# Kernel optimization log

Measured on AMD Instinct MI355X. Metric: run time of the kernel, lower is better.

## Reference

```python
import jax, jax.numpy as jnp
import numpy as np

N_HEAD, D_MODEL, D_K, D_V = 16, 1024, 64, 64
B, S = 4, 2048
LN_EPS = 1e-5

def setup_inputs() -> dict:
    key = jax.random.key(0)
    ks = jax.random.split(key, 12)
    s = 1.0 / np.sqrt(D_MODEL)
    x = jax.random.normal(ks[0], (B, S, D_MODEL), dtype=jnp.float32)
    Wq = jax.random.normal(ks[1], (N_HEAD, D_MODEL, D_K), dtype=jnp.float32) * s
    bq = jax.random.normal(ks[2], (N_HEAD, D_K), dtype=jnp.float32) * 0.01
    Wk = jax.random.normal(ks[3], (N_HEAD, D_MODEL, D_K), dtype=jnp.float32) * s
    bk = jax.random.normal(ks[4], (N_HEAD, D_K), dtype=jnp.float32) * 0.01
    Wv = jax.random.normal(ks[5], (N_HEAD, D_MODEL, D_V), dtype=jnp.float32) * s
    bv = jax.random.normal(ks[6], (N_HEAD, D_V), dtype=jnp.float32) * 0.01
    Wfc = jax.random.normal(ks[7], (N_HEAD * D_V, D_MODEL), dtype=jnp.float32) * (1.0 / np.sqrt(N_HEAD * D_V))
    bfc = jax.random.normal(ks[8], (D_MODEL,), dtype=jnp.float32) * 0.01
    gamma = jnp.ones((D_MODEL,), dtype=jnp.float32)
    beta = jnp.zeros((D_MODEL,), dtype=jnp.float32)
    return {"x": x, "Wq": Wq, "bq": bq, "Wk": Wk, "bk": bk, "Wv": Wv, "bv": bv,
            "Wfc": Wfc, "bfc": bfc, "gamma": gamma, "beta": beta}

def reference(x, Wq, bq, Wk, bk, Wv, bv, Wfc, bfc, gamma, beta):
    # Per-head projections batched over heads: [B,H,S,d]
    q = jnp.einsum('bsd,hdk->bhsk', x, Wq) + bq[None, :, None, :]
    k = jnp.einsum('bsd,hdk->bhsk', x, Wk) + bk[None, :, None, :]
    v = jnp.einsum('bsd,hdv->bhsv', x, Wv) + bv[None, :, None, :]
    scores = jnp.einsum('bhqk,bhsk->bhqs', q, k) / jnp.sqrt(jnp.float32(D_K))
    probs = jax.nn.softmax(scores, axis=-1)
    attn = jnp.einsum('bhqs,bhsv->bhqv', probs, v)  # [B,H,S,Dv]
    # concat heads (cat along last dim == transpose heads to feature axis)
    cat = attn.transpose(0, 2, 1, 3).reshape(B, S, N_HEAD * D_V)
    y = cat @ Wfc + bfc
    mu = jnp.mean(y, axis=-1, keepdims=True)
    var = jnp.mean(jnp.square(y - mu), axis=-1, keepdims=True)
    return (y - mu) * jax.lax.rsqrt(var + LN_EPS) * gamma + beta
```

## Files before the change

kernel.cpp:

```cpp
#include <hip/hip_runtime.h>

#define NH 16
#define DMODEL 1024
#define DK 64
#define DV 64
#define BB 4
#define SS 2048
#define NTOK (BB*SS)
#define LN_EPS 1e-5f
#define SM_SHIFT 13.0f

typedef __attribute__((ext_vector_type(4))) float f32x4;
typedef __attribute__((ext_vector_type(8))) short s16x8;
typedef __attribute__((ext_vector_type(4))) short s16x4;

__device__ __forceinline__ short f2bf(float f) {
    union { float f; unsigned u; } a; a.f = f;
    unsigned r = a.u + 0x7FFFu + ((a.u >> 16) & 1u);
    return (short)(r >> 16);
}
__device__ __forceinline__ unsigned pk2(float a, float b) {
    union { float f; unsigned u; } x, y; x.f = a; y.f = b;
    return __builtin_amdgcn_perm(x.u + 0x8000u, y.u + 0x8000u, 0x07060302u);
}
__device__ __forceinline__ float fexp2(float x) { return __builtin_amdgcn_exp2f(x); }
__device__ __forceinline__ void gll16(const void* g, void* l) {
    __builtin_amdgcn_global_load_lds(
        (const __attribute__((address_space(1))) unsigned int*)g,
        (__attribute__((address_space(3))) unsigned int*)l, 16, 0, 0);
}

__global__ void k_cast_x(const float* __restrict__ x, short* __restrict__ xb) {
    int i = blockIdx.x * blockDim.x + threadIdx.x;
    f32x4 v = reinterpret_cast<const f32x4*>(x)[i];
    s16x4 o;
    o[0] = f2bf(v[0]); o[1] = f2bf(v[1]); o[2] = f2bf(v[2]); o[3] = f2bf(v[3]);
    reinterpret_cast<s16x4*>(xb)[i] = o;
}

__global__ __launch_bounds__(256) void k_conv_wqkv_t(const float* __restrict__ Wq,
                                                     const float* __restrict__ Wk,
                                                     const float* __restrict__ Wv,
                                                     short* __restrict__ WT) {
    __shared__ float tile[64][17];
    const int mh = blockIdx.y;
    const int mat = mh >> 4, h = mh & 15;
    const int dt = blockIdx.x >> 2, kt = blockIdx.x & 3;
    const float* src = (mat == 0 ? Wq : (mat == 1 ? Wk : Wv));
    const int t = threadIdx.x;
    #pragma unroll
    for (int p = 0; p < 4; p++) {
        int d = p * 16 + (t >> 4), kk = t & 15;
        tile[d][kk] = src[((size_t)h * 1024 + dt * 64 + d) * 64 + kt * 16 + kk];
    }
    __syncthreads();
    #pragma unroll
    for (int p = 0; p < 4; p++) {
        int kk = p * 4 + (t >> 6), d = t & 63;
        WT[((size_t)mat * 1024 + h * 64 + kt * 16 + kk) * 1024 + dt * 64 + d] = f2bf(tile[d][kk]);
    }
}

__global__ __launch_bounds__(256) void k_conv_wfc_t(const float* __restrict__ Wfc,
                                                    short* __restrict__ WfcT) {
    __shared__ float tile[64][17];
    const int ct = blockIdx.x >> 6, nt = blockIdx.x & 63;
    const int t = threadIdx.x;
    #pragma unroll
    for (int p = 0; p < 4; p++) {
        int c = p * 16 + (t >> 4), n = t & 15;
        tile[c][n] = Wfc[((size_t)ct * 64 + c) * 1024 + nt * 16 + n];
    }
    __syncthreads();
    #pragma unroll
    for (int p = 0; p < 4; p++) {
        int n = p * 4 + (t >> 6), c = t & 63;
        WfcT[((size_t)nt * 16 + n) * 1024 + ct * 64 + c] = f2bf(tile[c][n]);
    }
}

template<int MODE, int NBX, int NWG>
__global__ __launch_bounds__(256) void k_gemm2(const short* __restrict__ A,
                                               const short* __restrict__ BT,
                                               const float* __restrict__ bq,
                                               const float* __restrict__ bk,
                                               const float* __restrict__ bv,
                                               const float* __restrict__ bfc,
                                               short* __restrict__ Qb,
                                               short* __restrict__ Kb,
                                               short* __restrict__ Vt,
                                               short* __restrict__ Yb) {
    __shared__ short smem[2][128][64];
    const int fid = blockIdx.x + blockIdx.y * NBX;
    const int swzid = (fid & 7) * (NWG / 8) + (fid >> 3);
    const int gm0 = (swzid / NBX) * 128, gn0 = (swzid % NBX) * 128;
    const int t = threadIdx.x, lane = t & 63, w = t >> 6;
    const int wm = w >> 1, wn = w & 1;
    const int lr = lane & 15, lg = lane >> 4;

    f32x4 acc[4][4] = {};

    const int lrow = t >> 3, gl = t & 7;
    const int sgx = (gl ^ (lrow & 7)) << 3;
    const short* pa = A  + (size_t)(gm0 + lrow) * 1024 + sgx;
    const short* pb = BT + (size_t)(gn0 + lrow) * 1024 + sgx;
    char* dA = (char*)smem[0] + w * 1024;
    char* dB = (char*)smem[1] + w * 1024;

    const int x7 = lr & 7;
    const int gx0 = (lg ^ x7) << 4;
    const int gx1 = ((4 + lg) ^ x7) << 4;

    for (int k0 = 0; k0 < 1024; k0 += 64) {
        #pragma unroll
        for (int c = 0; c < 4; c++) {
            gll16(pa + (size_t)c * 32768 + k0, dA + c * 4096);
            gll16(pb + (size_t)c * 32768 + k0, dB + c * 4096);
        }
        __syncthreads();
        s16x8 aF[2][4], bF[2][4];
        #pragma unroll
        for (int i = 0; i < 4; i++) {
            const char* rpa = (char*)smem[0] + (wm * 64 + i * 16 + lr) * 128;
            const char* rpb = (char*)smem[1] + (wn * 64 + i * 16 + lr) * 128;
            aF[0][i] = *(const s16x8*)(rpa + gx0);
            aF[1][i] = *(const s16x8*)(rpa + gx1);
            bF[0][i] = *(const s16x8*)(rpb + gx0);
            bF[1][i] = *(const s16x8*)(rpb + gx1);
        }
        __builtin_amdgcn_s_setprio(1);
        #pragma unroll
        for (int kk = 0; kk < 2; kk++)
            #pragma unroll
            for (int i = 0; i < 4; i++)
                #pragma unroll
                for (int j = 0; j < 4; j++)
                    acc[i][j] = __builtin_amdgcn_mfma_f32_16x16x32_bf16(aF[kk][i], bF[kk][j], acc[i][j], 0, 0, 0);
        __builtin_amdgcn_s_setprio(0);
        __syncthreads();
    }

    short (*ct)[128] = (short(*)[128])smem;
    const float* bias; int nloc0; float scale = 1.0f;
    if (MODE == 0) {
        if (gn0 < 1024)      { bias = bq; nloc0 = gn0;        scale = 0.18033688011112042f; }
        else if (gn0 < 2048) { bias = bk; nloc0 = gn0 - 1024; }
        else                 { bias = bv; nloc0 = gn0 - 2048; }
    } else { bias = bfc; nloc0 = gn0; }
    float bval[4];
    #pragma unroll
    for (int j = 0; j < 4; j++) bval[j] = bias[nloc0 + wn * 64 + j * 16 + lr];

    #pragma unroll
    for (int i = 0; i < 4; i++)
        #pragma unroll
        for (int j = 0; j < 4; j++) {
            const int colg = wn * 4 + j;
            #pragma unroll
            for (int rg = 0; rg < 4; rg++) {
                int row = wm * 64 + i * 16 + lg * 4 + rg;
                int cg = colg ^ ((row >> 1) & 7);
                ct[row][(cg << 4) + lr] = f2bf((acc[i][j][rg] + bval[j]) * scale);
            }
        }
    __syncthreads();

    if (MODE == 0 && gn0 >= 2048) {
        const int s0 = gm0 & 2047;
        const int b2v = gm0 >> 11;
        const int cg16 = lane >> 4;
        const int l16 = lane & 15;
        #pragma unroll
        for (int step = 0; step < 8; step++) {
            int c = w * 32 + step * 4 + cg16;
            int nl = (gn0 - 2048) + c;
            int h2 = nl >> 6, v = nl & 63;
            s16x8 o;
            #pragma unroll
            for (int j = 0; j < 8; j++) {
                int p = l16 * 8 + j;
                int blk = p >> 5, g = (p >> 3) & 3, h16 = (p >> 2) & 1, i2 = p & 3;
                int row = blk * 32 + h16 * 16 + g * 4 + i2;
                int cg2 = (c >> 4) ^ ((row >> 1) & 7);
                o[j] = ct[row][(cg2 << 4) + (c & 15)];
            }
            *(s16x8*)(Vt + ((size_t)(b2v * NH + h2) * 64 + v) * SS + s0 + l16 * 8) = o;
        }
    } else {
        short* dstM = (MODE == 0) ? (gn0 < 1024 ? Qb : Kb) : Yb;
        #pragma unroll
        for (int rr = 0; rr < 2; rr++) {
            const int row = w * 16 + (lane >> 2) + rr * 64;
            const int m = gm0 + row;
            const int swz = (row >> 1) & 7;
            #pragma unroll
            for (int j = 0; j < 4; j++) {
                const int c = (lane & 3) + j * 4;
                const int cg = (c >> 1) ^ swz;
                s16x8 v = *(const s16x8*)((char*)ct + row * 256 + (cg << 5) + (c & 1) * 16);
                if (MODE == 0) {
                    int b2 = m >> 11, s2 = m & 2047;
                    int n0 = (gn0 & 1023) + c * 8;
                    int h2 = n0 >> 6, kk = n0 & 63;
                    *(s16x8*)(dstM + ((size_t)(b2 * NH + h2) * SS + s2) * DK + kk) = v;
                } else {
                    *(s16x8*)(dstM + (size_t)m * 1024 + gn0 + c * 8) = v;
                }
            }
        }
    }
}

__global__ __launch_bounds__(512) void k_attn2(const short* __restrict__ Qb,
                                               const short* __restrict__ Kb,
                                               const short* __restrict__ VT2,
                                               short* __restrict__ cat) {
    __shared__ char smem[2][16384];
    const int fid = blockIdx.x + blockIdx.y * gridDim.x;
    const int swz = ((fid & 7) << 6) | (fid >> 3);
    const int qt = swz & 7, bh = swz >> 3;
    const int b = bh >> 4, h = bh & 15;
    const int t = threadIdx.x, lane = t & 63, w = t >> 6;
    const int lr = lane & 15, lg = lane >> 4;

    const short* Qbase = Qb + ((size_t)bh * SS + qt * 256 + w * 32) * DK;
    s16x8 qF[2][2];
    #pragma unroll
    for (int f = 0; f < 2; f++) {
        qF[f][0] = *(const s16x8*)(Qbase + (f * 16 + lr) * DK + lg * 8);
        qF[f][1] = *(const s16x8*)(Qbase + (f * 16 + lr) * DK + 32 + lg * 8);
    }
    s16x8 onesF;
    #pragma unroll
    for (int i = 0; i < 8; i++) onesF[i] = (short)0x3F80;

    const char* Kbase = (const char*)(Kb + (size_t)bh * SS * DK);
    const char* Vbase = (const char*)(VT2 + (size_t)bh * DK * SS);
    const int rk = w * 8 + (lane >> 3);
    const int gl = lane & 7;
    const char* pK = Kbase + rk * 128 + ((gl ^ (rk & 7)) << 4);
    const char* pV = Vbase + rk * (SS * 2) + ((gl ^ (rk & 7)) << 4);

    const int x7 = lr & 7;
    const int gx0 = (lg ^ x7) << 4;
    const int gx1 = ((4 + lg) ^ x7) << 4;

    f32x4 acc[2][4] = {};
    f32x4 accs[2] = {};
    const f32x4 zinit = {-SM_SHIFT, -SM_SHIFT, -SM_SHIFT, -SM_SHIFT};

    {
        char* d = smem[0];
        gll16(pK, d + w * 1024);
        gll16(pV, d + 8192 + w * 1024);
    }
    __syncthreads();

    int cur = 0;
    for (int kt = 0; kt < SS; kt += 64) {
        if (kt + 64 < SS) {
            char* d = smem[cur ^ 1];
            gll16(pK + (kt + 64) * 128, d + w * 1024);
            gll16(pV + (kt + 64) * 2,   d + 8192 + w * 1024);
        }
        const char* bs = smem[cur];

        s16x8 kA[4][2];
        #pragma unroll
        for (int kg = 0; kg < 4; kg++) {
            const char* rp = bs + (kg * 16 + lr) * 128;
            kA[kg][0] = *(const s16x8*)(rp + gx0);
            kA[kg][1] = *(const s16x8*)(rp + gx1);
        }
        f32x4 st[2][4];
        __builtin_amdgcn_s_setprio(1);
        #pragma unroll
        for (int f = 0; f < 2; f++)
            #pragma unroll
            for (int kg = 0; kg < 4; kg++) {
                f32x4 z = __builtin_amdgcn_mfma_f32_16x16x32_bf16(kA[kg][0], qF[f][0], zinit, 0, 0, 0);
                st[f][kg] = __builtin_amdgcn_mfma_f32_16x16x32_bf16(kA[kg][1], qF[f][1], z, 0, 0, 0);
            }
        __builtin_amdgcn_s_setprio(0);

        s16x8 pb[2][2];
        #pragma unroll
        for (int f = 0; f < 2; f++) {
            float p[4][4];
            #pragma unroll
            for (int kg = 0; kg < 4; kg++)
                #pragma unroll
                for (int rg = 0; rg < 4; rg++)
                    p[kg][rg] = fexp2(st[f][kg][rg]);
            #pragma unroll
            for (int ks = 0; ks < 2; ks++) {
                union { s16x8 v; unsigned u[4]; } U;
                U.u[0] = pk2(p[2 * ks][1],     p[2 * ks][0]);
                U.u[1] = pk2(p[2 * ks][3],     p[2 * ks][2]);
                U.u[2] = pk2(p[2 * ks + 1][1], p[2 * ks + 1][0]);
                U.u[3] = pk2(p[2 * ks + 1][3], p[2 * ks + 1][2]);
                pb[f][ks] = U.v;
            }
        }

        __builtin_amdgcn_s_setprio(1);
        #pragma unroll
        for (int f = 0; f < 2; f++) {
            accs[f] = __builtin_amdgcn_mfma_f32_16x16x32_bf16(onesF, pb[f][0], accs[f], 0, 0, 0);
            accs[f] = __builtin_amdgcn_mfma_f32_16x16x32_bf16(onesF, pb[f][1], accs[f], 0, 0, 0);
        }
        #pragma unroll
        for (int vt = 0; vt < 4; vt++) {
            const char* rp = bs + 8192 + (vt * 16 + lr) * 128;
            s16x8 vA0 = *(const s16x8*)(rp + gx0);
            s16x8 vA1 = *(const s16x8*)(rp + gx1);
            #pragma unroll
            for (int f = 0; f < 2; f++) {
                acc[f][vt] = __builtin_amdgcn_mfma_f32_16x16x32_bf16(vA0, pb[f][0], acc[f][vt], 0, 0, 0);
                acc[f][vt] = __builtin_amdgcn_mfma_f32_16x16x32_bf16(vA1, pb[f][1], acc[f][vt], 0, 0, 0);
            }
        }
        __builtin_amdgcn_s_setprio(0);
        __syncthreads();
        cur ^= 1;
    }

    char* ods = (char*)smem + w * 4096;
    float inv[2] = {1.0f / accs[0][0], 1.0f / accs[1][0]};
    #pragma unroll
    for (int f = 0; f < 2; f++)
        #pragma unroll
        for (int vt = 0; vt < 4; vt++)
            #pragma unroll
            for (int rg = 0; rg < 4; rg++)
                *(short*)(ods + (f * 16 + lr) * 128 + (vt * 16 + lg * 4 + rg) * 2) =
                    f2bf(acc[f][vt][rg] * inv[f]);
    __syncthreads();
    {
        int r = lane >> 1, hb = lane & 1;
        const char* srow = (char*)smem + w * 4096 + r * 128 + hb * 64;
        int token = b * SS + qt * 256 + w * 32 + r;
        char* dst = (char*)(cat + (size_t)token * 1024 + h * 64 + hb * 32);
        #pragma unroll
        for (int i = 0; i < 4; i++)
            *(s16x8*)(dst + i * 16) = *(const s16x8*)(srow + i * 16);
    }
}

__global__ __launch_bounds__(256) void k_ln(const short* __restrict__ Yb,
                                            const float* __restrict__ gamma,
                                            const float* __restrict__ beta,
                                            float* __restrict__ out) {
    const int row = blockIdx.x;
    const int t = threadIdx.x;
    s16x4 raw = reinterpret_cast<const s16x4*>(Yb + (size_t)row * 1024)[t];
    float v[4];
    #pragma unroll
    for (int i = 0; i < 4; i++) {
        union { unsigned u; float f; } cvt;
        cvt.u = ((unsigned)(unsigned short)raw[i]) << 16;
        v[i] = cvt.f;
    }
    float s = v[0] + v[1] + v[2] + v[3];
    float s2 = v[0] * v[0] + v[1] * v[1] + v[2] * v[2] + v[3] * v[3];
    #pragma unroll
    for (int off = 32; off; off >>= 1) {
        s += __shfl_xor(s, off);
        s2 += __shfl_xor(s2, off);
    }
    __shared__ float red[8];
    int w = t >> 6, lane = t & 63;
    if (lane == 0) { red[w] = s; red[4 + w] = s2; }
    __syncthreads();
    float S = red[0] + red[1] + red[2] + red[3];
    float S2 = red[4] + red[5] + red[6] + red[7];
    float mu = S * (1.f / 1024.f);
    float var = S2 * (1.f / 1024.f) - mu * mu;
    float rs = rsqrtf(var + LN_EPS);
    f32x4 g = reinterpret_cast<const f32x4*>(gamma)[t];
    f32x4 be = reinterpret_cast<const f32x4*>(beta)[t];
    f32x4 o;
    #pragma unroll
    for (int i = 0; i < 4; i++) o[i] = (v[i] - mu) * rs * g[i] + be[i];
    reinterpret_cast<f32x4*>(out + (size_t)row * 1024)[t] = o;
}

extern "C" void kernel_launch(void* const* d_in, const int* in_sizes, int n_in,
                              void* d_out, int out_size, void* d_ws, size_t ws_size,
                              hipStream_t stream) {
    const float* x    = (const float*)d_in[0];
    const float* Wq   = (const float*)d_in[1];
    const float* bq   = (const float*)d_in[2];
    const float* Wk   = (const float*)d_in[3];
    const float* bk   = (const float*)d_in[4];
    const float* Wv   = (const float*)d_in[5];
    const float* bv   = (const float*)d_in[6];
    const float* Wfc  = (const float*)d_in[7];
    const float* bfc  = (const float*)d_in[8];
    const float* gamma= (const float*)d_in[9];
    const float* beta = (const float*)d_in[10];
    float* out = (float*)d_out;

    char* p = (char*)d_ws;
    short* xb   = (short*)p; p += (size_t)NTOK * 1024 * 2;
    short* WT   = (short*)p; p += (size_t)3072 * 1024 * 2;
    short* WfcT = (short*)p; p += (size_t)1024 * 1024 * 2;
    short* Qb   = (short*)p; p += (size_t)64 * SS * 64 * 2;
    short* Kb   = (short*)p; p += (size_t)64 * SS * 64 * 2;
    short* Vb   = (short*)p; p += (size_t)64 * SS * 64 * 2;
    short* VTb  = (short*)p; p += (size_t)64 * 64 * SS * 2;
    short* cat  = (short*)p; p += (size_t)NTOK * 1024 * 2;
    short* Yb   = Qb;
    (void)Vb;

    k_cast_x     <<<NTOK * 1024 / 4 / 256, 256, 0, stream>>>(x, xb);
    k_conv_wqkv_t<<<dim3(64, 48), 256, 0, stream>>>(Wq, Wk, Wv, WT);
    k_conv_wfc_t <<<1024, 256, 0, stream>>>(Wfc, WfcT);
    k_gemm2<0, 24, 1536><<<dim3(24, 64), 256, 0, stream>>>(xb, WT, bq, bk, bv, nullptr, Qb, Kb, VTb, nullptr);
    k_attn2      <<<dim3(8, 64), 512, 0, stream>>>(Qb, Kb, VTb, cat);
    k_gemm2<1, 8, 512><<<dim3(8, 64), 256, 0, stream>>>(cat, WfcT, nullptr, nullptr, nullptr, bfc, nullptr, nullptr, nullptr, Yb);
    k_ln         <<<NTOK, 256, 0, stream>>>(Yb, gamma, beta, out);
}
```

Before: 183.9 us.

## Halve per-wave query rows in attention kernel and double the grid

Each wave in the attention kernel now processes 16 query rows instead of 32, so a block covers 128 queries and the grid doubles to 1024 blocks. This cuts accumulator and score registers per wave and gives more blocks to spread across the CUs, aiming for better occupancy and load balance. In exchange, K/V tiles are loaded from global/LDS twice as often per query, which lowers data reuse.

New measurement: 192.1 us. 4.5% more time.

```diff
diff --git a/kernel.cpp b/kernel.cpp
--- a/kernel.cpp
+++ b/kernel.cpp
@@ -217,19 +217,15 @@
                                                short* __restrict__ cat) {
     __shared__ char smem[2][16384];
     const int fid = blockIdx.x + blockIdx.y * gridDim.x;
-    const int swz = ((fid & 7) << 6) | (fid >> 3);
-    const int qt = swz & 7, bh = swz >> 3;
+    const int swz = ((fid & 7) << 7) | (fid >> 3);
+    const int qt = swz & 15, bh = swz >> 4;
     const int b = bh >> 4, h = bh & 15;
     const int t = threadIdx.x, lane = t & 63, w = t >> 6;
     const int lr = lane & 15, lg = lane >> 4;
 
-    const short* Qbase = Qb + ((size_t)bh * SS + qt * 256 + w * 32) * DK;
-    s16x8 qF[2][2];
-    #pragma unroll
-    for (int f = 0; f < 2; f++) {
-        qF[f][0] = *(const s16x8*)(Qbase + (f * 16 + lr) * DK + lg * 8);
-        qF[f][1] = *(const s16x8*)(Qbase + (f * 16 + lr) * DK + 32 + lg * 8);
-    }
+    const short* Qbase = Qb + ((size_t)bh * SS + qt * 128 + w * 16) * DK;
+    s16x8 qF0 = *(const s16x8*)(Qbase + lr * DK + lg * 8);
+    s16x8 qF1 = *(const s16x8*)(Qbase + lr * DK + 32 + lg * 8);
     s16x8 onesF;
     #pragma unroll
     for (int i = 0; i < 8; i++) onesF[i] = (short)0x3F80;
@@ -245,8 +241,8 @@
     const int gx0 = (lg ^ x7) << 4;
     const int gx1 = ((4 + lg) ^ x7) << 4;
 
-    f32x4 acc[2][4] = {};
-    f32x4 accs[2] = {};
+    f32x4 acc[4] = {};
+    f32x4 accs = {};
     const f32x4 zinit = {-SM_SHIFT, -SM_SHIFT, -SM_SHIFT, -SM_SHIFT};
 
     {
@@ -272,78 +268,63 @@
             kA[kg][0] = *(const s16x8*)(rp + gx0);
             kA[kg][1] = *(const s16x8*)(rp + gx1);
         }
-        f32x4 st[2][4];
+        f32x4 st[4];
         __builtin_amdgcn_s_setprio(1);
         #pragma unroll
-        for (int f = 0; f < 2; f++)
+        for (int kg = 0; kg < 4; kg++) {
+            f32x4 z = __builtin_amdgcn_mfma_f32_16x16x32_bf16(kA[kg][0], qF0, zinit, 0, 0, 0);
+            st[kg] = __builtin_amdgcn_mfma_f32_16x16x32_bf16(kA[kg][1], qF1, z, 0, 0, 0);
+        }
+        __builtin_amdgcn_s_setprio(0);
+
+        float p[4][4];
+        #pragma unroll
+        for (int kg = 0; kg < 4; kg++)
             #pragma unroll
-            for (int kg = 0; kg < 4; kg++) {
-                f32x4 z = __builtin_amdgcn_mfma_f32_16x16x32_bf16(kA[kg][0], qF[f][0], zinit, 0, 0, 0);
-                st[f][kg] = __builtin_amdgcn_mfma_f32_16x16x32_bf16(kA[kg][1], qF[f][1], z, 0, 0, 0);
-            }
-        __builtin_amdgcn_s_setprio(0);
-
-        s16x8 pb[2][2];
-        #pragma unroll
-        for (int f = 0; f < 2; f++) {
-            float p[4][4];
-            #pragma unroll
-            for (int kg = 0; kg < 4; kg++)
-                #pragma unroll
-                for (int rg = 0; rg < 4; rg++)
-                    p[kg][rg] = fexp2(st[f][kg][rg]);
-            #pragma unroll
-            for (int ks = 0; ks < 2; ks++) {
-                union { s16x8 v; unsigned u[4]; } U;
-                U.u[0] = pk2(p[2 * ks][1],     p[2 * ks][0]);
-                U.u[1] = pk2(p[2 * ks][3],     p[2 * ks][2]);
-                U.u[2] = pk2(p[2 * ks + 1][1], p[2 * ks + 1][0]);
-                U.u[3] = pk2(p[2 * ks + 1][3], p[2 * ks + 1][2]);
-                pb[f][ks] = U.v;
-            }
+            for (int rg = 0; rg < 4; rg++)
+                p[kg][rg] = fexp2(st[kg][rg]);
+        s16x8 pb[2];
+        #pragma unroll
+        for (int ks = 0; ks < 2; ks++) {
+            union { s16x8 v; unsigned u[4]; } U;
+            U.u[0] = pk2(p[2 * ks][1],     p[2 * ks][0]);
+            U.u[1] = pk2(p[2 * ks][3],     p[2 * ks][2]);
+            U.u[2] = pk2(p[2 * ks + 1][1], p[2 * ks + 1][0]);
+            U.u[3] = pk2(p[2 * ks + 1][3], p[2 * ks + 1][2]);
+            pb[ks] = U.v;
         }
 
         __builtin_amdgcn_s_setprio(1);
-        #pragma unroll
-        for (int f = 0; f < 2; f++) {
-            accs[f] = __builtin_amdgcn_mfma_f32_16x16x32_bf16(onesF, pb[f][0], accs[f], 0, 0, 0);
-            accs[f] = __builtin_amdgcn_mfma_f32_16x16x32_bf16(onesF, pb[f][1], accs[f], 0, 0, 0);
-        }
+        accs = __builtin_amdgcn_mfma_f32_16x16x32_bf16(onesF, pb[0], accs, 0, 0, 0);
+        accs = __builtin_amdgcn_mfma_f32_16x16x32_bf16(onesF, pb[1], accs, 0, 0, 0);
         #pragma unroll
         for (int vt = 0; vt < 4; vt++) {
             const char* rp = bs + 8192 + (vt * 16 + lr) * 128;
             s16x8 vA0 = *(const s16x8*)(rp + gx0);
             s16x8 vA1 = *(const s16x8*)(rp + gx1);
-            #pragma unroll
-            for (int f = 0; f < 2; f++) {
-                acc[f][vt] = __builtin_amdgcn_mfma_f32_16x16x32_bf16(vA0, pb[f][0], acc[f][vt], 0, 0, 0);
-                acc[f][vt] = __builtin_amdgcn_mfma_f32_16x16x32_bf16(vA1, pb[f][1], acc[f][vt], 0, 0, 0);
-            }
+            acc[vt] = __builtin_amdgcn_mfma_f32_16x16x32_bf16(vA0, pb[0], acc[vt], 0, 0, 0);
+            acc[vt] = __builtin_amdgcn_mfma_f32_16x16x32_bf16(vA1, pb[1], acc[vt], 0, 0, 0);
         }
         __builtin_amdgcn_s_setprio(0);
         __syncthreads();
         cur ^= 1;
     }
 
-    char* ods = (char*)smem + w * 4096;
-    float inv[2] = {1.0f / accs[0][0], 1.0f / accs[1][0]};
-    #pragma unroll
-    for (int f = 0; f < 2; f++)
-        #pragma unroll
-        for (int vt = 0; vt < 4; vt++)
-            #pragma unroll
-            for (int rg = 0; rg < 4; rg++)
-                *(short*)(ods + (f * 16 + lr) * 128 + (vt * 16 + lg * 4 + rg) * 2) =
-                    f2bf(acc[f][vt][rg] * inv[f]);
+    char* ods = (char*)smem + w * 2048;
+    float inv = 1.0f / accs[0];
+    #pragma unroll
+    for (int vt = 0; vt < 4; vt++)
+        #pragma unroll
+        for (int rg = 0; rg < 4; rg++)
+            *(short*)(ods + lr * 128 + (vt * 16 + lg * 4 + rg) * 2) = f2bf(acc[vt][rg] * inv);
     __syncthreads();
     {
-        int r = lane >> 1, hb = lane & 1;
-        const char* srow = (char*)smem + w * 4096 + r * 128 + hb * 64;
-        int token = b * SS + qt * 256 + w * 32 + r;
-        char* dst = (char*)(cat + (size_t)token * 1024 + h * 64 + hb * 32);
-        #pragma unroll
-        for (int i = 0; i < 4; i++)
-            *(s16x8*)(dst + i * 16) = *(const s16x8*)(srow + i * 16);
+        int r = lane >> 2, hb = lane & 3;
+        const char* srow = (char*)smem + w * 2048 + r * 128 + hb * 32;
+        int token = b * SS + qt * 128 + w * 16 + r;
+        char* dst = (char*)(cat + (size_t)token * 1024 + h * 64 + hb * 16);
+        *(s16x8*)(dst)      = *(const s16x8*)(srow);
+        *(s16x8*)(dst + 16) = *(const s16x8*)(srow + 16);
     }
 }
 
@@ -417,7 +398,7 @@
     k_conv_wqkv_t<<<dim3(64, 48), 256, 0, stream>>>(Wq, Wk, Wv, WT);
     k_conv_wfc_t <<<1024, 256, 0, stream>>>(Wfc, WfcT);
     k_gemm2<0, 24, 1536><<<dim3(24, 64), 256, 0, stream>>>(xb, WT, bq, bk, bv, nullptr, Qb, Kb, VTb, nullptr);
-    k_attn2      <<<dim3(8, 64), 512, 0, stream>>>(Qb, Kb, VTb, cat);
+    k_attn2      <<<dim3(16, 64), 512, 0, stream>>>(Qb, Kb, VTb, cat);
     k_gemm2<1, 8, 512><<<dim3(8, 64), 256, 0, stream>>>(cat, WfcT, nullptr, nullptr, nullptr, bfc, nullptr, nullptr, nullptr, Yb);
     k_ln         <<<NTOK, 256, 0, stream>>>(Yb, gamma, beta, out);
 }
```

## Split QKV projection into 256x256-tile GEMM for Q/K and existing kernel for V

Applied to the files above, without the earlier changes.

The Q and K columns of the fused QKV projection move to a new 512-thread GEMM that uses 256x256 output tiles, explicit double-buffered LDS staging with direct global-to-LDS loads, and MFMA priority hints. The V part stays on the old 128x128 kernel, now launched with a column offset so it writes the transposed V layout. Larger tiles are meant to raise arithmetic intensity and cut global traffic for the Q/K projection. The cost is an extra kernel launch, higher LDS and register pressure, and fewer workgroups for the Q/K part (256 blocks).

After: 179.4 us. -2.4%, faster.

```diff
diff --git a/kernel.cpp b/kernel.cpp
--- a/kernel.cpp
+++ b/kernel.cpp
@@ -79,7 +79,139 @@
     }
 }
 
-template<int MODE, int NBX, int NWG>
+__global__ __launch_bounds__(512, 2) void k_gemm3(const short* __restrict__ A,
+                                                  const short* __restrict__ BT,
+                                                  const float* __restrict__ bq,
+                                                  const float* __restrict__ bk,
+                                                  short* __restrict__ Qb,
+                                                  short* __restrict__ Kb) {
+    __shared__ short lds[2][2][256][64];
+    const int fid = blockIdx.x + blockIdx.y * 8;
+    const int swz = (fid & 7) * 32 + (fid >> 3);
+    const int gm0 = (swz >> 3) * 256, gn0 = (swz & 7) * 256;
+    const int t = threadIdx.x, lane = t & 63, w = t >> 6;
+    const int wm = w >> 2, wn = w & 3;
+    const int lr = lane & 15, lg = lane >> 4;
+
+    f32x4 acc[8][4] = {};
+
+    const int lrow = t >> 3, gl = t & 7;
+    const int sgx = (gl ^ (lrow & 7)) << 3;
+    const short* pa = A  + (size_t)(gm0 + lrow) * 1024 + sgx;
+    const short* pb = BT + (size_t)(gn0 + lrow) * 1024 + sgx;
+
+    const int x7 = lr & 7;
+    const int gx0 = (lg ^ x7) << 4;
+    const int gx1 = ((4 + lg) ^ x7) << 4;
+
+    char* a0 = (char*)lds[0][0]; char* b0 = (char*)lds[0][1];
+    char* a1 = (char*)lds[1][0]; char* b1 = (char*)lds[1][1];
+
+    auto STAGE = [&](int k0, char* dA, char* dB) {
+        #pragma unroll
+        for (int c = 0; c < 4; c++) {
+            gll16(pa + (size_t)c * 65536 + k0, dA + c * 8192 + t * 16);
+            gll16(pb + (size_t)c * 65536 + k0, dB + c * 8192 + t * 16);
+        }
+    };
+    auto COMPUTE = [&](const char* bA, const char* bB) {
+        s16x8 bF[4][2];
+        #pragma unroll
+        for (int n = 0; n < 4; n++) {
+            const char* rp = bB + (wn * 64 + n * 16 + lr) * 128;
+            bF[n][0] = *(const s16x8*)(rp + gx0);
+            bF[n][1] = *(const s16x8*)(rp + gx1);
+        }
+        #pragma unroll
+        for (int ph = 0; ph < 4; ph++) {
+            s16x8 aF[2][2];
+            #pragma unroll
+            for (int mm = 0; mm < 2; mm++) {
+                const char* rp = bA + (wm * 128 + (ph * 2 + mm) * 16 + lr) * 128;
+                aF[mm][0] = *(const s16x8*)(rp + gx0);
+                aF[mm][1] = *(const s16x8*)(rp + gx1);
+            }
+            __builtin_amdgcn_s_setprio(1);
+            #pragma unroll
+            for (int ks = 0; ks < 2; ks++)
+                #pragma unroll
+                for (int mm = 0; mm < 2; mm++)
+                    #pragma unroll
+                    for (int n = 0; n < 4; n++)
+                        acc[ph * 2 + mm][n] = __builtin_amdgcn_mfma_f32_16x16x32_bf16(
+                            aF[mm][ks], bF[n][ks], acc[ph * 2 + mm][n], 0, 0, 0);
+            __builtin_amdgcn_s_setprio(0);
+        }
+    };
+
+    STAGE(0, a0, b0);
+    #pragma unroll 1
+    for (int kt2 = 0; kt2 < 8; kt2++) {
+        STAGE((2 * kt2 + 1) * 64, a1, b1);
+        asm volatile("s_waitcnt vmcnt(8)" ::: "memory");
+        __builtin_amdgcn_s_barrier();
+        __builtin_amdgcn_sched_barrier(0);
+        COMPUTE(a0, b0);
+        __builtin_amdgcn_sched_barrier(0);
+        __builtin_amdgcn_s_barrier();
+        if (kt2 < 7) {
+            STAGE((2 * kt2 + 2) * 64, a0, b0);
+            asm volatile("s_waitcnt vmcnt(8)" ::: "memory");
+        } else {
+            asm volatile("s_waitcnt vmcnt(0)" ::: "memory");
+        }
+        __builtin_amdgcn_s_barrier();
+        __builtin_amdgcn_sched_barrier(0);
+        COMPUTE(a1, b1);
+        __builtin_amdgcn_sched_barrier(0);
+        __builtin_amdgcn_s_barrier();
+    }
+
+    short (*ct)[256] = (short(*)[256])lds;
+    const float* bias = (gn0 < 1024) ? bq : bk;
+    const int nloc0 = gn0 & 1023;
+    const float scale = (gn0 < 1024) ? 0.18033688011112042f : 1.0f;
+    float bval[4];
+    #pragma unroll
+    for (int n = 0; n < 4; n++) bval[n] = bias[nloc0 + wn * 64 + n * 16 + lr];
+
+    #pragma unroll
+    for (int m = 0; m < 8; m++)
+        #pragma unroll
+        for (int n = 0; n < 4; n++) {
+            const int colg = wn * 4 + n;
+            #pragma unroll
+            for (int rg = 0; rg < 4; rg++) {
+                int row = wm * 128 + m * 16 + lg * 4 + rg;
+                int cg = colg ^ ((row << 1) & 15);
+                ct[row][(cg << 4) + lr] = f2bf((acc[m][n][rg] + bval[n]) * scale);
+            }
+        }
+    __syncthreads();
+
+    short* dstM = (gn0 < 1024) ? Qb : Kb;
+    const int qm = w >> 2, w4 = w & 3;
+    #pragma unroll
+    for (int qn = 0; qn < 2; qn++)
+        #pragma unroll
+        for (int rr = 0; rr < 2; rr++) {
+            const int row = qm * 128 + w4 * 16 + (lane >> 2) + rr * 64;
+            const int m = gm0 + row;
+            const int b2 = m >> 11, s2 = m & 2047;
+            #pragma unroll
+            for (int j = 0; j < 4; j++) {
+                const int cl = (lane & 3) + j * 4;
+                const int chunk = qn * 16 + cl;
+                const int cgs = (chunk >> 1) ^ ((row << 1) & 15);
+                s16x8 v = *(const s16x8*)((char*)ct + row * 512 + (cgs << 5) + (chunk & 1) * 16);
+                const int n0 = nloc0 + qn * 128 + cl * 8;
+                const int h2 = n0 >> 6, kk = n0 & 63;
+                *(s16x8*)(dstM + ((size_t)(b2 * NH + h2) * SS + s2) * DK + kk) = v;
+            }
+        }
+}
+
+template<int MODE, int NBX, int NWG, int GOFF>
 __global__ __launch_bounds__(256) void k_gemm2(const short* __restrict__ A,
                                                const short* __restrict__ BT,
                                                const float* __restrict__ bq,
@@ -93,7 +225,7 @@
     __shared__ short smem[2][128][64];
     const int fid = blockIdx.x + blockIdx.y * NBX;
     const int swzid = (fid & 7) * (NWG / 8) + (fid >> 3);
-    const int gm0 = (swzid / NBX) * 128, gn0 = (swzid % NBX) * 128;
+    const int gm0 = (swzid / NBX) * 128, gn0 = (swzid % NBX) * 128 + GOFF;
     const int t = threadIdx.x, lane = t & 63, w = t >> 6;
     const int wm = w >> 1, wn = w & 1;
     const int lr = lane & 15, lg = lane >> 4;
@@ -165,7 +297,7 @@
         }
     __syncthreads();
 
-    if (MODE == 0 && gn0 >= 2048) {
+    if (MODE == 0 && GOFF >= 2048) {
         const int s0 = gm0 & 2047;
         const int b2v = gm0 >> 11;
         const int cg16 = lane >> 4;
@@ -416,8 +548,9 @@
     k_cast_x     <<<NTOK * 1024 / 4 / 256, 256, 0, stream>>>(x, xb);
     k_conv_wqkv_t<<<dim3(64, 48), 256, 0, stream>>>(Wq, Wk, Wv, WT);
     k_conv_wfc_t <<<1024, 256, 0, stream>>>(Wfc, WfcT);
-    k_gemm2<0, 24, 1536><<<dim3(24, 64), 256, 0, stream>>>(xb, WT, bq, bk, bv, nullptr, Qb, Kb, VTb, nullptr);
+    k_gemm3      <<<dim3(8, 32), 512, 0, stream>>>(xb, WT, bq, bk, Qb, Kb);
+    k_gemm2<0, 8, 512, 2048><<<dim3(8, 64), 256, 0, stream>>>(xb, WT, bq, bk, bv, nullptr, Qb, Kb, VTb, nullptr);
     k_attn2      <<<dim3(8, 64), 512, 0, stream>>>(Qb, Kb, VTb, cat);
-    k_gemm2<1, 8, 512><<<dim3(8, 64), 256, 0, stream>>>(cat, WfcT, nullptr, nullptr, nullptr, bfc, nullptr, nullptr, nullptr, Yb);
+    k_gemm2<1, 8, 512, 0><<<dim3(8, 64), 256, 0, stream>>>(cat, WfcT, nullptr, nullptr, nullptr, bfc, nullptr, nullptr, nullptr, Yb);
     k_ln         <<<NTOK, 256, 0, stream>>>(Yb, gamma, beta, out);
 }
```
